# Kernel tuning notes

Measured on AMD Instinct MI355X. Metric: run time of the kernel, lower is better.

## Reference

```python
import jax, jax.numpy as jnp
import numpy as np

EPS = 1e-5
B, T, D, V, NB, C, R, MT = 2, 256, 2048, 32000, 4, 512, 32, 3


def ste_sign_vec(w):
    alpha = jnp.mean(jnp.abs(w))
    hard = alpha * jnp.sign(w)
    hard = jnp.where(hard == 0, alpha, hard)
    return w + jax.lax.stop_gradient(hard - w)


def ste_sign(w):
    alpha = jnp.mean(jnp.abs(w), axis=-1, keepdims=True)
    hard = alpha * jnp.sign(w)
    hard = jnp.where(hard == 0, alpha, hard)
    return w + jax.lax.stop_gradient(hard - w)


def layernorm(x, g, b):
    m = jnp.mean(x, axis=-1, keepdims=True)
    v = jnp.var(x, axis=-1, keepdims=True)
    return (x - m) * jax.lax.rsqrt(v + EPS) * g + b


def hdc_block(x, i, decay_logit, bv_q, bv_k, bv_v, rules, query_bind, logic_gate,
              ln_mem_g, ln_mem_b, ln_attn_g, ln_attn_b, ln_logic_g, ln_logic_b,
              ctrl_ln_g, ctrl_ln_b, down_w, down_b, up_w, up_b):
    t = jnp.arange(T)
    # --- EMA memory (conv1d with decay^k kernel == lower-tri decay matmul) ---
    decay = jax.nn.sigmoid(decay_logit[i])
    expnt = t[:, None] - t[None, :]                     # (T,T)
    A = jnp.where(expnt >= 0, decay ** jnp.maximum(expnt, 0).astype(x.dtype), 0.0)
    mem = jnp.einsum('ts,bsd->btd', A, x)
    x = layernorm(x + mem, ln_mem_g[i], ln_mem_b[i])
    # --- sigmoid-gated boolean causal attention ---
    Q = x * ste_sign_vec(bv_q[i])
    K = x * ste_sign_vec(bv_k[i])
    Vv = x * ste_sign_vec(bv_v[i])
    scores = jnp.einsum('btd,bsd->bts', Q, K) * (D ** -0.5)
    causal = t[:, None] >= t[None, :]
    attn = jnp.where(causal[None], jax.nn.sigmoid(scores * 4.0), 0.0)
    att_out = jnp.einsum('bts,bsd->btd', attn, Vv)
    x = layernorm(x + att_out, ln_attn_g[i], ln_attn_b[i])
    # --- logic layer: sum_r w_r * (x*rule_r) == x * (w @ rules) ---
    rls = ste_sign(rules[i])                            # (R,D)
    query = x * ste_sign_vec(query_bind[i])
    sim = jnp.einsum('btd,rd->btr', query, rls) * (D ** -0.5)
    rw = jax.nn.sigmoid(sim * 4.0)
    logic_out = x * jnp.einsum('btr,rd->btd', rw, rls)
    gate = jax.nn.sigmoid(logic_gate[i])
    x = layernorm(x + gate * (logic_out - x), ln_logic_g[i], ln_logic_b[i])
    # --- controller MLP (dropout inactive in eval) ---
    h = layernorm(x, ctrl_ln_g[i], ctrl_ln_b[i])
    h = jax.nn.gelu(h @ down_w[i].T + down_b[i], approximate=False)
    h = h @ up_w[i].T + up_b[i]
    return x + h


def setup_inputs() -> dict:
    key = jax.random.key(0)
    ks = jax.random.split(key, 12)
    nrm = jax.random.normal
    return {
        'idx': jax.random.randint(ks[0], (B, T), 0, V),
        'codebook': 0.02 * nrm(ks[1], (V, D)),
        'decay_logit': jnp.full((NB,), 2.0),
        'bv_q': 0.5 * nrm(ks[2], (NB, D)),
        'bv_k': 0.5 * nrm(ks[3], (NB, D)),
        'bv_v': 0.5 * nrm(ks[4], (NB, D)),
        'rules': 0.5 * nrm(ks[5], (NB, R, D)),
        'query_bind': 0.5 * nrm(ks[6], (NB, D)),
        'logic_gate': jnp.full((NB,), -1.0),
        'ln_mem_g': jnp.ones((NB, D)), 'ln_mem_b': jnp.zeros((NB, D)),
        'ln_attn_g': jnp.ones((NB, D)), 'ln_attn_b': jnp.zeros((NB, D)),
        'ln_logic_g': jnp.ones((NB, D)), 'ln_logic_b': jnp.zeros((NB, D)),
        'ctrl_ln_g': jnp.ones((NB, D)), 'ctrl_ln_b': jnp.zeros((NB, D)),
        'down_w': nrm(ks[7], (NB, C, D)) / np.sqrt(D), 'down_b': jnp.zeros((NB, C)),
        'up_w': nrm(ks[8], (NB, D, C)) / np.sqrt(C), 'up_b': jnp.zeros((NB, D)),
        'tl_gates': jnp.zeros((MT,)),
        'tl_pos': 0.01 * nrm(ks[9], (MT, D)),
        'tl_ln_g': jnp.ones((D,)), 'tl_ln_b': jnp.zeros((D,)),
        'out_ln_g': jnp.ones((D,)), 'out_ln_b': jnp.zeros((D,)),
        'output_scale': jnp.array(1.0),
    }


def reference(idx, codebook, decay_logit, bv_q, bv_k, bv_v, rules, query_bind,
              logic_gate, ln_mem_g, ln_mem_b, ln_attn_g, ln_attn_b, ln_logic_g,
              ln_logic_b, ctrl_ln_g, ctrl_ln_b, down_w, down_b, up_w, up_b,
              tl_gates, tl_pos, tl_ln_g, tl_ln_b, out_ln_g, out_ln_b, output_scale):
    blk = (decay_logit, bv_q, bv_k, bv_v, rules, query_bind, logic_gate,
           ln_mem_g, ln_mem_b, ln_attn_g, ln_attn_b, ln_logic_g, ln_logic_b,
           ctrl_ln_g, ctrl_ln_b, down_w, down_b, up_w, up_b)

    def run_blocks(h):
        for i in range(NB):
            h = hdc_block(h, i, *blk)
        return h

    # encode: STE bipolar codebook + cyclic permutation positional binding
    tokens = ste_sign(jnp.take(codebook, idx, axis=0))  # (B,T,D)
    perm = (jnp.arange(D)[None, :] - jnp.arange(T)[:, None]) % D  # (T,D)
    tokens = jnp.take_along_axis(tokens, jnp.broadcast_to(perm[None], tokens.shape), axis=2)

    h = run_blocks(tokens)
    for ti in range(1, MT):  # thought loop (n_thoughts = max_thoughts)
        gate = jax.nn.sigmoid(tl_gates[ti])
        thought = run_blocks(layernorm(h, tl_ln_g, tl_ln_b) + tl_pos[ti])
        h = h + gate * (thought - h)

    h = layernorm(h, out_ln_g, out_ln_b)
    logits = (h @ codebook.T) * output_scale  # (B,T,V) weight-tied decoder
    return logits
```

## Files before the change

### kernel.cpp

```cpp
#include <hip/hip_runtime.h>
#include <math.h>

#define TT   256
#define DD   2048
#define VV   32000
#define NBLK 4
#define CC   512
#define RR   32
#define MTT  3
#define NBAT 2
#define NTOK 512

typedef unsigned int u32;
typedef unsigned short ushort_t;
typedef __attribute__((ext_vector_type(8))) short s16x8;
typedef __attribute__((ext_vector_type(4))) float f32x4;

__device__ __forceinline__ float sigm(float x){ return 1.0f/(1.0f+expf(-x)); }

__device__ __forceinline__ ushort_t f2bf(float f){
  u32 u = __float_as_uint(f);
  u32 r = (u + 0x7fffu + ((u >> 16) & 1u)) >> 16;
  return (ushort_t)r;
}
__device__ __forceinline__ float bf2f(ushort_t u){
  return __uint_as_float(((u32)u) << 16);
}

__device__ __forceinline__ void async_copy16(void* lds, const void* g){
  __builtin_amdgcn_global_load_lds((const __attribute__((address_space(1))) u32*)g,
                                   (__attribute__((address_space(3))) u32*)lds, 16, 0, 0);
}

__device__ __forceinline__ float block_sum256(float v){
  #pragma unroll
  for (int off = 32; off > 0; off >>= 1) v += __shfl_down(v, off);
  __shared__ float sh[4];
  __syncthreads();
  if ((threadIdx.x & 63) == 0) sh[threadIdx.x >> 6] = v;
  __syncthreads();
  return sh[0] + sh[1] + sh[2] + sh[3];
}

__global__ __launch_bounds__(256) void cvt2_kernel(const float* __restrict__ a,
    ushort_t* __restrict__ oa, long na4,
    const float* __restrict__ b, ushort_t* __restrict__ ob, long nb4){
  long i = (long)blockIdx.x * 256 + threadIdx.x;
  long stride = (long)gridDim.x * 256;
  long tot = na4 + nb4;
  for (; i < tot; i += stride){
    const float* src = (i < na4) ? a : b;
    ushort_t* dst = (i < na4) ? oa : ob;
    long k = (i < na4) ? i : i - na4;
    float4 v = ((const float4*)src)[k];
    ushort4 o;
    o.x = f2bf(v.x); o.y = f2bf(v.y); o.z = f2bf(v.z); o.w = f2bf(v.w);
    ((ushort4*)dst)[k] = o;
  }
}

__global__ __launch_bounds__(256) void sign_prep_kernel(
    const float* __restrict__ bv_q, const float* __restrict__ bv_k,
    const float* __restrict__ bv_v, const float* __restrict__ query_bind,
    const float* __restrict__ rules, const float* __restrict__ decay_logit,
    float* __restrict__ SQK, float* __restrict__ SV, float* __restrict__ SQB,
    ushort_t* __restrict__ RLSb, ushort_t* __restrict__ Adec){
  int b = blockIdx.x;
  if (b >= 3*NBLK + NBLK*RR){
    int e = b - (3*NBLK + NBLK*RR);
    int i = e >> 8, t = e & (TT - 1), s = threadIdx.x;
    float decay = sigm(decay_logit[i]);
    float l2 = log2f(decay);
    int ex = t - s;
    float v = (ex < 0) ? 0.f : exp2f((float)ex * l2);
    Adec[((size_t)i*TT + t)*TT + s] = f2bf(v);
    return;
  }
  if (b < NBLK){
    const float* q = bv_q + (size_t)b * DD;
    const float* k = bv_k + (size_t)b * DD;
    float sq = 0.f, sk = 0.f;
    #pragma unroll
    for (int j = 0; j < 8; j++){
      int d = threadIdx.x + j*256;
      sq += fabsf(q[d]); sk += fabsf(k[d]);
    }
    float aq = block_sum256(sq) * (1.f/DD);
    float ak = block_sum256(sk) * (1.f/DD);
    float a2 = aq * ak;
    float* o = SQK + (size_t)b * DD;
    #pragma unroll
    for (int j = 0; j < 8; j++){
      int d = threadIdx.x + j*256;
      o[d] = ((q[d] < 0.f) != (k[d] < 0.f)) ? -a2 : a2;
    }
    return;
  }
  const float* w; float* of = nullptr; ushort_t* ob = nullptr;
  if (b < 2*NBLK){ w = bv_v + (size_t)(b - NBLK) * DD; of = SV + (size_t)(b - NBLK) * DD; }
  else if (b < 3*NBLK){ w = query_bind + (size_t)(b - 2*NBLK) * DD; of = SQB + (size_t)(b - 2*NBLK) * DD; }
  else { int r = b - 3*NBLK; w = rules + (size_t)r * DD; ob = RLSb + (size_t)r * DD; }
  float s = 0.f;
  #pragma unroll
  for (int j = 0; j < 8; j++) s += fabsf(w[threadIdx.x + j*256]);
  float a = block_sum256(s) * (1.f/DD);
  #pragma unroll
  for (int j = 0; j < 8; j++){
    int d = threadIdx.x + j*256;
    float v = (w[d] < 0.f) ? -a : a;
    if (of) of[d] = v;
    else    ob[d] = f2bf(v);
  }
}

__global__ __launch_bounds__(256) void encode_kernel(const int* __restrict__ idx,
    const float* __restrict__ cb, float* __restrict__ X, ushort_t* __restrict__ Xrb){
  int token = blockIdx.x;
  int t = token & (TT - 1);
  size_t row = (size_t)idx[token] * DD;
  float s = 0.f;
  #pragma unroll
  for (int j = 0; j < 8; j++) s += fabsf(cb[row + threadIdx.x + j*256]);
  float a = block_sum256(s) * (1.f/DD);
  #pragma unroll
  for (int j = 0; j < 8; j++){
    int d = threadIdx.x + j*256;
    float w = cb[row + ((d - t) & (DD - 1))];
    float v = (w < 0.f) ? -a : a;
    X[(size_t)token * DD + d] = v;
    Xrb[(size_t)token * DD + d] = f2bf(v);
  }
}

__global__ __launch_bounds__(256) void ln_kernel(const float* __restrict__ A,
    const float* __restrict__ g, const float* __restrict__ be,
    float* __restrict__ out, ushort_t* __restrict__ outb,
    const float* __restrict__ qscale, ushort_t* __restrict__ outq,
    const float* __restrict__ vscale, ushort_t* __restrict__ outv){
  size_t row = blockIdx.x;
  const float* a = A + row * DD;
  int d0 = threadIdx.x * 8;
  float v[8];
  *(float4*)&v[0] = *(const float4*)(a + d0);
  *(float4*)&v[4] = *(const float4*)(a + d0 + 4);
  float s = 0.f, ss = 0.f;
  #pragma unroll
  for (int j = 0; j < 8; j++){ s += v[j]; ss += v[j]*v[j]; }
  float mean = block_sum256(s) * (1.f/DD);
  float var  = block_sum256(ss) * (1.f/DD) - mean*mean;
  float inv  = rsqrtf(var + 1e-5f);
  float gv[8], bv[8];
  *(float4*)&gv[0] = *(const float4*)(g + d0);
  *(float4*)&gv[4] = *(const float4*)(g + d0 + 4);
  *(float4*)&bv[0] = *(const float4*)(be + d0);
  *(float4*)&bv[4] = *(const float4*)(be + d0 + 4);
  float y[8];
  #pragma unroll
  for (int j = 0; j < 8; j++) y[j] = (v[j] - mean) * inv * gv[j] + bv[j];
  if (out){
    *(float4*)(out + row*DD + d0)     = *(float4*)&y[0];
    *(float4*)(out + row*DD + d0 + 4) = *(float4*)&y[4];
  }
  if (outb){
    s16x8 o;
    #pragma unroll
    for (int j = 0; j < 8; j++) o[j] = (short)f2bf(y[j]);
    *(s16x8*)(outb + row*DD + d0) = o;
  }
  if (outq){
    float qv[8];
    *(float4*)&qv[0] = *(const float4*)(qscale + d0);
    *(float4*)&qv[4] = *(const float4*)(qscale + d0 + 4);
    s16x8 o;
    #pragma unroll
    for (int j = 0; j < 8; j++) o[j] = (short)f2bf(y[j] * qv[j]);
    *(s16x8*)(outq + row*DD + d0) = o;
  }
  if (outv){
    float vv[8];
    *(float4*)&vv[0] = *(const float4*)(vscale + d0);
    *(float4*)&vv[4] = *(const float4*)(vscale + d0 + 4);
    s16x8 o;
    #pragma unroll
    for (int j = 0; j < 8; j++) o[j] = (short)f2bf(y[j] * vv[j]);
    *(s16x8*)(outv + row*DD + d0) = o;
  }
}

__global__ __launch_bounds__(256) void fuse_logic_kernel(const float* __restrict__ T0,
    const ushort_t* __restrict__ RLSi, const float* __restrict__ SQBi,
    const float* __restrict__ g2, const float* __restrict__ b2,
    const float* __restrict__ gate_ptr,
    const float* __restrict__ g3, const float* __restrict__ b3,
    const float* __restrict__ g4, const float* __restrict__ b4,
    float* __restrict__ X, ushort_t* __restrict__ T1b){
  __shared__ float sh[256*33];
  __shared__ float red[8*32];
  __shared__ float rwsh[32];
  const float RSD = 0.022097086912079608f;
  int tid = threadIdx.x;
  size_t tok = blockIdx.x;
  const float* a = T0 + tok * DD;
  int d0 = tid * 8;
  float v[8];
  *(float4*)&v[0] = *(const float4*)(a + d0);
  *(float4*)&v[4] = *(const float4*)(a + d0 + 4);
  float s = 0.f, ss = 0.f;
  #pragma unroll
  for (int j = 0; j < 8; j++){ s += v[j]; ss += v[j]*v[j]; }
  float mean = block_sum256(s) * (1.f/DD);
  float var  = block_sum256(ss) * (1.f/DD) - mean*mean;
  float inv  = rsqrtf(var + 1e-5f);
  float g2v[8], b2v[8], sqv[8];
  *(float4*)&g2v[0] = *(const float4*)(g2 + d0);
  *(float4*)&g2v[4] = *(const float4*)(g2 + d0 + 4);
  *(float4*)&b2v[0] = *(const float4*)(b2 + d0);
  *(float4*)&b2v[4] = *(const float4*)(b2 + d0 + 4);
  *(float4*)&sqv[0] = *(const float4*)(SQBi + d0);
  *(float4*)&sqv[4] = *(const float4*)(SQBi + d0 + 4);
  float y2[8], xq[8];
  #pragma unroll
  for (int j = 0; j < 8; j++){
    y2[j] = (v[j] - mean) * inv * g2v[j] + b2v[j];
    xq[j] = y2[j] * sqv[j];
  }
  float aa[32];
  #pragma unroll 4
  for (int r = 0; r < 32; r++){
    s16x8 rv = *(const s16x8*)(RLSi + (size_t)r*DD + d0);
    float t = 0.f;
    #pragma unroll
    for (int j = 0; j < 8; j++)
      t = fmaf(xq[j], bf2f((ushort_t)rv[j]), t);
    aa[r] = t;
  }
  #pragma unroll
  for (int r = 0; r < 32; r++) sh[tid*33 + r] = aa[r];
  __syncthreads();
  {
    int r = tid & 31, gg = tid >> 5;
    float t = 0.f;
    #pragma unroll 8
    for (int i = 0; i < 32; i++) t += sh[(gg*32 + i)*33 + r];
    red[gg*32 + r] = t;
  }
  __syncthreads();
  if (tid < 32){
    float t = 0.f;
    #pragma unroll
    for (int gg = 0; gg < 8; gg++) t += red[gg*32 + tid];
    rwsh[tid] = sigm(4.f * RSD * t);
  }
  __syncthreads();
  float gate = sigm(*gate_ptr);
  float acc8[8] = {};
  #pragma unroll 4
  for (int r = 0; r < 32; r++){
    s16x8 rv = *(const s16x8*)(RLSi + (size_t)r*DD + d0);
    float w = rwsh[r];
    #pragma unroll
    for (int j = 0; j < 8; j++)
      acc8[j] = fmaf(w, bf2f((ushort_t)rv[j]), acc8[j]);
  }
  float p3[8]; s = 0.f; ss = 0.f;
  #pragma unroll
  for (int j = 0; j < 8; j++){
    float lo = y2[j] * acc8[j];
    p3[j] = y2[j] + gate * (lo - y2[j]);
    s += p3[j]; ss += p3[j]*p3[j];
  }
  mean = block_sum256(s) * (1.f/DD);
  var  = block_sum256(ss) * (1.f/DD) - mean*mean;
  inv  = rsqrtf(var + 1e-5f);
  float g3v[8], b3v[8];
  *(float4*)&g3v[0] = *(const float4*)(g3 + d0);
  *(float4*)&g3v[4] = *(const float4*)(g3 + d0 + 4);
  *(float4*)&b3v[0] = *(const float4*)(b3 + d0);
  *(float4*)&b3v[4] = *(const float4*)(b3 + d0 + 4);
  float y3[8]; s = 0.f; ss = 0.f;
  #pragma unroll
  for (int j = 0; j < 8; j++){
    y3[j] = (p3[j] - mean) * inv * g3v[j] + b3v[j];
    s += y3[j]; ss += y3[j]*y3[j];
  }
  *(float4*)(X + tok*DD + d0)     = *(float4*)&y3[0];
  *(float4*)(X + tok*DD + d0 + 4) = *(float4*)&y3[4];
  mean = block_sum256(s) * (1.f/DD);
  var  = block_sum256(ss) * (1.f/DD) - mean*mean;
  inv  = rsqrtf(var + 1e-5f);
  float g4v[8], b4v[8];
  *(float4*)&g4v[0] = *(const float4*)(g4 + d0);
  *(float4*)&g4v[4] = *(const float4*)(g4 + d0 + 4);
  *(float4*)&b4v[0] = *(const float4*)(b4 + d0);
  *(float4*)&b4v[4] = *(const float4*)(b4 + d0 + 4);
  s16x8 o;
  #pragma unroll
  for (int j = 0; j < 8; j++)
    o[j] = (short)f2bf((y3[j] - mean) * inv * g4v[j] + b4v[j]);
  *(s16x8*)(T1b + tok*DD + d0) = o;
}

__global__ __launch_bounds__(256) void tl_kernel(const float* __restrict__ Xr,
    float* __restrict__ H, const float* __restrict__ gate_ptr,
    const float* __restrict__ g, const float* __restrict__ be,
    const float* __restrict__ pos,
    float* __restrict__ outX, ushort_t* __restrict__ outXb){
  size_t row = blockIdx.x;
  float gate = gate_ptr ? sigm(*gate_ptr) : 1.f;
  int d0 = threadIdx.x * 8;
  float xr[8];
  *(float4*)&xr[0] = *(const float4*)(Xr + row*DD + d0);
  *(float4*)&xr[4] = *(const float4*)(Xr + row*DD + d0 + 4);
  float v[8]; float s = 0.f, ss = 0.f;
  if (gate_ptr){
    float hv[8];
    *(float4*)&hv[0] = *(const float4*)(H + row*DD + d0);
    *(float4*)&hv[4] = *(const float4*)(H + row*DD + d0 + 4);
    #pragma unroll
    for (int j = 0; j < 8; j++) v[j] = hv[j] + gate * (xr[j] - hv[j]);
  } else {
    #pragma unroll
    for (int j = 0; j < 8; j++) v[j] = xr[j];
  }
  *(float4*)(H + row*DD + d0)     = *(float4*)&v[0];
  *(float4*)(H + row*DD + d0 + 4) = *(float4*)&v[4];
  #pragma unroll
  for (int j = 0; j < 8; j++){ s += v[j]; ss += v[j]*v[j]; }
  float mean = block_sum256(s) * (1.f/DD);
  float var  = block_sum256(ss) * (1.f/DD) - mean*mean;
  float inv  = rsqrtf(var + 1e-5f);
  float gv[8], bv[8];
  *(float4*)&gv[0] = *(const float4*)(g + d0);
  *(float4*)&gv[4] = *(const float4*)(g + d0 + 4);
  *(float4*)&bv[0] = *(const float4*)(be + d0);
  *(float4*)&bv[4] = *(const float4*)(be + d0 + 4);
  float y[8];
  #pragma unroll
  for (int j = 0; j < 8; j++) y[j] = (v[j] - mean) * inv * gv[j] + bv[j];
  if (pos){
    float pv[8];
    *(float4*)&pv[0] = *(const float4*)(pos + d0);
    *(float4*)&pv[4] = *(const float4*)(pos + d0 + 4);
    #pragma unroll
    for (int j = 0; j < 8; j++) y[j] += pv[j];
  }
  if (outX){
    *(float4*)(outX + row*DD + d0)     = *(float4*)&y[0];
    *(float4*)(outX + row*DD + d0 + 4) = *(float4*)&y[4];
  }
  if (outXb){
    s16x8 o;
    #pragma unroll
    for (int j = 0; j < 8; j++) o[j] = (short)f2bf(y[j]);
    *(s16x8*)(outXb + row*DD + d0) = o;
  }
}

template<int BM, int BN, int SPLITK, int ACT, bool CAUSAL, bool OUTBF>
__global__ __launch_bounds__(256) void gemm_nt(const ushort_t* __restrict__ A,
    const ushort_t* __restrict__ B, void* __restrict__ Cv,
    int K, int lda, int ldb, int ldc,
    long sA, long sB, long sC,
    const float* __restrict__ colscale, const float* __restrict__ bias,
    const float* __restrict__ res, ushort_t* __restrict__ mirror,
    const float* __restrict__ alpha_ptr, float alpha_c)
{
  constexpr int FM = BM / 32;
  constexpr int FN = BN / 32;
  __shared__ __align__(16) ushort_t shA[BM * 64];
  __shared__ __align__(16) ushort_t shB[BN * 64];
  const int tid = threadIdx.x;
  const int l = tid & 63, w = tid >> 6;
  const int wr = w >> 1, wc = w & 1;
  const int row0 = blockIdx.y * BM, col0 = blockIdx.x * BN;
  const int zb = blockIdx.z / SPLITK, zk = blockIdx.z % SPLITK;

  if (CAUSAL && col0 > row0 + BM - 1) return;

  A += (size_t)zb * sA;
  B += (size_t)zb * sB;
  const int kbeg = zk * (K / SPLITK), kend = kbeg + K / SPLITK;

  f32x4 acc[FM][FN] = {};

  for (int kt = kbeg; kt < kend; kt += 64){
    #pragma unroll
    for (int i = 0; i < BM/32; i++){
      int o = i*4096 + tid*16;
      int r = o >> 7, c = (o >> 4) & 7;
      int lc = c ^ (r & 7);
      async_copy16((char*)shA + o, A + (size_t)(row0 + r) * lda + kt + lc*8);
    }
    #pragma unroll
    for (int i = 0; i < BN/32; i++){
      int o = i*4096 + tid*16;
      int r = o >> 7, c = (o >> 4) & 7;
      int lc = c ^ (r & 7);
      async_copy16((char*)shB + o, B + (size_t)(col0 + r) * ldb + kt + lc*8);
    }
    __syncthreads();
    #pragma unroll
    for (int kk = 0; kk < 2; kk++){
      s16x8 af[FM], bfr[FN];
      #pragma unroll
      for (int mi = 0; mi < FM; mi++){
        int r = wr*(BM/2) + mi*16 + (l & 15);
        int c = kk*4 + (l >> 4);
        af[mi] = *(const s16x8*)((const char*)shA + r*128 + ((c ^ (r & 7)) << 4));
      }
      #pragma unroll
      for (int ni = 0; ni < FN; ni++){
        int r = wc*(BN/2) + ni*16 + (l & 15);
        int c = kk*4 + (l >> 4);
        bfr[ni] = *(const s16x8*)((const char*)shB + r*128 + ((c ^ (r & 7)) << 4));
      }
      #pragma unroll
      for (int mi = 0; mi < FM; mi++)
        #pragma unroll
        for (int ni = 0; ni < FN; ni++)
          acc[mi][ni] = __builtin_amdgcn_mfma_f32_16x16x32_bf16(af[mi], bfr[ni], acc[mi][ni], 0, 0, 0);
    }
    __syncthreads();
  }

  if (SPLITK > 1){
    float* P = (float*)Cv + (size_t)blockIdx.z * sC;
    #pragma unroll
    for (int mi = 0; mi < FM; mi++)
      #pragma unroll
      for (int ni = 0; ni < FN; ni++)
        #pragma unroll
        for (int j = 0; j < 4; j++){
          int m = row0 + wr*(BM/2) + mi*16 + (l >> 4)*4 + j;
          int n = col0 + wc*(BN/2) + ni*16 + (l & 15);
          P[(size_t)m * ldc + n] = acc[mi][ni][j];
        }
    return;
  }

  float alpha = alpha_c * (alpha_ptr ? *alpha_ptr : 1.f);
  float* Cf = (float*)Cv + (size_t)zb * sC;
  ushort_t* Cb = (ushort_t*)Cv + (size_t)zb * sC;
  const float* resz = res ? res + (size_t)zb * sC : nullptr;
  #pragma unroll
  for (int mi = 0; mi < FM; mi++){
    #pragma unroll
    for (int ni = 0; ni < FN; ni++){
      #pragma unroll
      for (int j = 0; j < 4; j++){
        int m = row0 + wr*(BM/2) + mi*16 + (l >> 4)*4 + j;
        int n = col0 + wc*(BN/2) + ni*16 + (l & 15);
        float v = acc[mi][ni][j] * alpha;
        if (colscale) v *= colscale[n];
        if (bias) v += bias[n];
        if (ACT == 1) v = sigm(4.f * v);
        else if (ACT == 2) v = 0.5f * v * (1.f + erff(v * 0.70710678118654752f));
        if (CAUSAL && n > m) v = 0.f;
        if (resz) v += resz[(size_t)m * ldc + n];
        if (OUTBF) Cb[(size_t)m * ldc + n] = f2bf(v);
        else       Cf[(size_t)m * ldc + n] = v;
        if (mirror) mirror[(size_t)m * ldc + n] = f2bf(v);
      }
    }
  }
}

__global__ __launch_bounds__(256) void gemm_nn(const ushort_t* __restrict__ A,
    const ushort_t* __restrict__ B, float* __restrict__ C,
    int K, int lda, int ldb, int ldc,
    long sA, long sB, long sC,
    const float* __restrict__ res, int tri)
{
  __shared__ __align__(16) ushort_t shA[64 * 64];
  __shared__ __align__(16) ushort_t shB[64 * 64];
  const int tid = threadIdx.x;
  const int l = tid & 63, w = tid >> 6;
  const int wr = w >> 1, wc = w & 1;
  const int row0 = blockIdx.y * 64, col0 = blockIdx.x * 64;
  A += (size_t)blockIdx.z * sA;
  B += (size_t)blockIdx.z * sB;

  const int kb = tid & 63;
  const int nb0 = (tid >> 6) * 8;
  const int kend = tri ? (row0 + 64 < K ? row0 + 64 : K) : K;

  f32x4 acc[2][2] = {};

  for (int kt = 0; kt < kend; kt += 64){
    #pragma unroll
    for (int i = 0; i < 2; i++){
      int o = i*4096 + tid*16;
      int r = o >> 7, c = (o >> 4) & 7;
      int lc = c ^ (r & 7);
      async_copy16((char*)shA + o, A + (size_t)(row0 + r) * lda + kt + lc*8);
    }
    #pragma unroll
    for (int i = 0; i < 2; i++){
      int n0 = nb0 + i*32;
      s16x8 v = *(const s16x8*)(B + (size_t)(kt + kb) * ldb + col0 + n0);
      #pragma unroll
      for (int j = 0; j < 8; j++){
        int n = n0 + j;
        int off = n*128 + (((kb >> 3) ^ (n & 7)) << 4) + ((kb & 7) << 1);
        *(ushort_t*)((char*)shB + off) = (ushort_t)v[j];
      }
    }
    __syncthreads();
    #pragma unroll
    for (int kk = 0; kk < 2; kk++){
      s16x8 af[2], bfr[2];
      #pragma unroll
      for (int mi = 0; mi < 2; mi++){
        int r = wr*32 + mi*16 + (l & 15);
        int c = kk*4 + (l >> 4);
        af[mi] = *(const s16x8*)((const char*)shA + r*128 + ((c ^ (r & 7)) << 4));
      }
      #pragma unroll
      for (int ni = 0; ni < 2; ni++){
        int r = wc*32 + ni*16 + (l & 15);
        int c = kk*4 + (l >> 4);
        bfr[ni] = *(const s16x8*)((const char*)shB + r*128 + ((c ^ (r & 7)) << 4));
      }
      #pragma unroll
      for (int mi = 0; mi < 2; mi++)
        #pragma unroll
        for (int ni = 0; ni < 2; ni++)
          acc[mi][ni] = __builtin_amdgcn_mfma_f32_16x16x32_bf16(af[mi], bfr[ni], acc[mi][ni], 0, 0, 0);
    }
    __syncthreads();
  }

  float* Cf = C + (size_t)blockIdx.z * sC;
  const float* resz = res ? res + (size_t)blockIdx.z * sC : nullptr;
  #pragma unroll
  for (int mi = 0; mi < 2; mi++)
    #pragma unroll
    for (int ni = 0; ni < 2; ni++)
      #pragma unroll
      for (int j = 0; j < 4; j++){
        int m = row0 + wr*32 + mi*16 + (l >> 4)*4 + j;
        int n = col0 + wc*32 + ni*16 + (l & 15);
        float v = acc[mi][ni][j];
        if (resz) v += resz[(size_t)m * ldc + n];
        Cf[(size_t)m * ldc + n] = v;
      }
}

template<int S, int ACT, bool CAUSAL, bool OUTBF>
__global__ __launch_bounds__(256) void reduce_epi(const float* __restrict__ P,
    void* __restrict__ outv, int M, int N, const float* __restrict__ bias, float alpha){
  long MN = (long)M * N;
  long idx = ((long)blockIdx.x * 256 + threadIdx.x) * 4;
  int b = (int)(idx / MN);
  long r = idx - (long)b * MN;
  int m = (int)(r / N), n = (int)(r % N);
  if (CAUSAL && n > m){
    if (OUTBF){ ushort4 z = {0,0,0,0}; *(ushort4*)&((ushort_t*)outv)[(long)b*MN + r] = z; }
    else      { float4 z = {0.f,0.f,0.f,0.f}; *(float4*)&((float*)outv)[(long)b*MN + r] = z; }
    return;
  }
  float vv[4] = {0.f, 0.f, 0.f, 0.f};
  #pragma unroll
  for (int s = 0; s < S; s++){
    float4 p = *(const float4*)&P[((long)(b*S + s)) * MN + r];
    vv[0] += p.x; vv[1] += p.y; vv[2] += p.z; vv[3] += p.w;
  }
  ushort4 ob; float4 of;
  float* po = (float*)&of;
  ushort_t* pb = (ushort_t*)&ob;
  #pragma unroll
  for (int j = 0; j < 4; j++){
    float v = vv[j] * alpha;
    if (bias) v += bias[n + j];
    if (ACT == 1) v = sigm(4.f * v);
    else if (ACT == 2) v = 0.5f * v * (1.f + erff(v * 0.70710678118654752f));
    if (CAUSAL && n + j > m) v = 0.f;
    po[j] = v; pb[j] = f2bf(v);
  }
  if (OUTBF) *(ushort4*)&((ushort_t*)outv)[(long)b*MN + r] = ob;
  else       *(float4*)&((float*)outv)[(long)b*MN + r] = of;
}

__global__ __launch_bounds__(256) void gemm_ntf(const ushort_t* __restrict__ A,
    const float* __restrict__ B, float* __restrict__ C,
    const float* __restrict__ alpha_ptr)
{
  constexpr int BM = 256, BN = 64, FM = 8, FN = 2;
  constexpr int NXB = VV / BN;
  __shared__ __align__(16) ushort_t shA[BM * 64];
  __shared__ __align__(16) ushort_t shB[BN * 64];
  const int tid = threadIdx.x;
  const int l = tid & 63, w = tid >> 6;
  const int wr = w >> 1, wc = w & 1;
  int bid = blockIdx.x;
  int swz = (bid & 7) * 125 + (bid >> 3);
  int bx = swz % NXB, by = swz / NXB;
  const int row0 = by * BM, col0 = bx * BN;

  f32x4 acc[FM][FN] = {};

  for (int kt = 0; kt < DD; kt += 64){
    #pragma unroll
    for (int i = 0; i < FM; i++){
      int o = i*4096 + tid*16;
      int r = o >> 7, c = (o >> 4) & 7;
      int lc = c ^ (r & 7);
      async_copy16((char*)shA + o, A + (size_t)(row0 + r) * DD + kt + lc*8);
    }
    #pragma unroll
    for (int i = 0; i < 4; i++){
      int idx4 = tid + i*256;
      int r = idx4 >> 4, kq = idx4 & 15;
      float4 v = *(const float4*)(B + (size_t)(col0 + r) * DD + kt + kq*4);
      u32 p0 = ((u32)f2bf(v.y) << 16) | (u32)f2bf(v.x);
      u32 p1 = ((u32)f2bf(v.w) << 16) | (u32)f2bf(v.z);
      int off = r*128 + (((kq >> 1) ^ (r & 7)) << 4) + ((kq & 1) << 3);
      uint2 pp; pp.x = p0; pp.y = p1;
      *(uint2*)((char*)shB + off) = pp;
    }
    __syncthreads();
    #pragma unroll
    for (int kk = 0; kk < 2; kk++){
      s16x8 af[FM], bfr[FN];
      #pragma unroll
      for (int mi = 0; mi < FM; mi++){
        int r = wr*(BM/2) + mi*16 + (l & 15);
        int c = kk*4 + (l >> 4);
        af[mi] = *(const s16x8*)((const char*)shA + r*128 + ((c ^ (r & 7)) << 4));
      }
      #pragma unroll
      for (int ni = 0; ni < FN; ni++){
        int r = wc*(BN/2) + ni*16 + (l & 15);
        int c = kk*4 + (l >> 4);
        bfr[ni] = *(const s16x8*)((const char*)shB + r*128 + ((c ^ (r & 7)) << 4));
      }
      #pragma unroll
      for (int mi = 0; mi < FM; mi++)
        #pragma unroll
        for (int ni = 0; ni < FN; ni++)
          acc[mi][ni] = __builtin_amdgcn_mfma_f32_16x16x32_bf16(af[mi], bfr[ni], acc[mi][ni], 0, 0, 0);
    }
    __syncthreads();
  }

  float alpha = *alpha_ptr;
  #pragma unroll
  for (int mi = 0; mi < FM; mi++)
    #pragma unroll
    for (int ni = 0; ni < FN; ni++)
      #pragma unroll
      for (int j = 0; j < 4; j++){
        int m = row0 + wr*(BM/2) + mi*16 + (l >> 4)*4 + j;
        int n = col0 + wc*(BN/2) + ni*16 + (l & 15);
        C[(size_t)m * VV + n] = acc[mi][ni][j] * alpha;
      }
}

extern "C" void kernel_launch(void* const* d_in, const int* in_sizes, int n_in,
                              void* d_out, int out_size, void* d_ws, size_t ws_size,
                              hipStream_t stream){
  const int*   idx        = (const int*)  d_in[0];
  const float* cb         = (const float*)d_in[1];
  const float* decay_lg   = (const float*)d_in[2];
  const float* bv_q       = (const float*)d_in[3];
  const float* bv_k       = (const float*)d_in[4];
  const float* bv_v       = (const float*)d_in[5];
  const float* rules      = (const float*)d_in[6];
  const float* query_bind = (const float*)d_in[7];
  const float* logic_gate = (const float*)d_in[8];
  const float* ln_mem_g   = (const float*)d_in[9];
  const float* ln_mem_b   = (const float*)d_in[10];
  const float* ln_attn_g  = (const float*)d_in[11];
  const float* ln_attn_b  = (const float*)d_in[12];
  const float* ln_logic_g = (const float*)d_in[13];
  const float* ln_logic_b = (const float*)d_in[14];
  const float* ctrl_g     = (const float*)d_in[15];
  const float* ctrl_b     = (const float*)d_in[16];
  const float* down_w     = (const float*)d_in[17];
  const float* down_b     = (const float*)d_in[18];
  const float* up_w       = (const float*)d_in[19];
  const float* up_b       = (const float*)d_in[20];
  const float* tl_gates   = (const float*)d_in[21];
  const float* tl_pos     = (const float*)d_in[22];
  const float* tl_g       = (const float*)d_in[23];
  const float* tl_b       = (const float*)d_in[24];
  const float* out_g      = (const float*)d_in[25];
  const float* out_b      = (const float*)d_in[26];
  const float* oscale     = (const float*)d_in[27];
  float* out = (float*)d_out;

  const size_t ND = (size_t)NTOK * DD;
  char* p = (char*)d_ws;
  auto alloc = [&](size_t bytes){ void* r = p; p += (bytes + 255) & ~(size_t)255; return r; };
  float*    X       = (float*)   alloc(ND * 4);
  float*    H       = (float*)   alloc(ND * 4);
  float*    T0      = (float*)   alloc(ND * 4);
  ushort_t* Xrb     = (ushort_t*)alloc(ND * 2);
  ushort_t* Xb      = (ushort_t*)alloc(ND * 2);
  ushort_t* Xqb     = (ushort_t*)alloc(ND * 2);
  ushort_t* Xvb     = (ushort_t*)alloc(ND * 2);
  ushort_t* T1b     = (ushort_t*)alloc(ND * 2);
  ushort_t* ATTNb   = (ushort_t*)alloc((size_t)NBAT * TT * TT * 2);
  ushort_t* CBbuf   = (ushort_t*)alloc((size_t)NTOK * CC * 2);
  float*    PP      = (float*)   alloc((size_t)8 * NTOK * CC * 4);
  float*    SQK     = (float*)   alloc((size_t)NBLK * DD * 4);
  float*    SV      = (float*)   alloc((size_t)NBLK * DD * 4);
  float*    SQB     = (float*)   alloc((size_t)NBLK * DD * 4);
  ushort_t* RLSb    = (ushort_t*)alloc((size_t)NBLK * RR * DD * 2);
  ushort_t* Adec    = (ushort_t*)alloc((size_t)NBLK * TT * TT * 2);
  ushort_t* down_wb = (ushort_t*)alloc((size_t)NBLK * CC * DD * 2);
  ushort_t* up_wb   = (ushort_t*)alloc((size_t)NBLK * DD * CC * 2);

  const float RSD = 0.022097086912079608f;

  sign_prep_kernel<<<3*NBLK + NBLK*RR + NBLK*TT, 256, 0, stream>>>(
      bv_q, bv_k, bv_v, query_bind, rules, decay_lg, SQK, SV, SQB, RLSb, Adec);
  cvt2_kernel<<<2048, 256, 0, stream>>>(down_w, down_wb, (long)NBLK*CC*DD/4,
                                        up_w, up_wb, (long)NBLK*DD*CC/4);
  encode_kernel<<<NTOK, 256, 0, stream>>>(idx, cb, X, Xrb);

  auto run_blocks = [&](){
    for (int i = 0; i < NBLK; i++){
      const size_t iD = (size_t)i * DD;
      gemm_nn<<<dim3(DD/64, TT/64, NBAT), 256, 0, stream>>>(
          Adec + (size_t)i*TT*TT, Xrb, T0, TT, TT, DD, DD,
          0, (long)TT*DD, (long)TT*DD, X, 1);
      ln_kernel<<<NTOK, 256, 0, stream>>>(T0, ln_mem_g + iD, ln_mem_b + iD,
          X, Xb, SQK + iD, Xqb, SV + iD, Xvb);
      gemm_nt<64,64,8,0,true,false><<<dim3(TT/64, TT/64, NBAT*8), 256, 0, stream>>>(
          Xqb, Xb, PP, DD, DD, DD, TT,
          (long)TT*DD, (long)TT*DD, (long)TT*TT,
          nullptr, nullptr, nullptr, nullptr, nullptr, 1.f);
      reduce_epi<8,1,true,true><<<(NBAT*TT*TT)/1024, 256, 0, stream>>>(
          PP, ATTNb, TT, TT, nullptr, RSD);
      gemm_nn<<<dim3(DD/64, TT/64, NBAT), 256, 0, stream>>>(
          ATTNb, Xvb, T0, TT, TT, DD, DD,
          (long)TT*TT, (long)TT*DD, (long)TT*DD, X, 1);
      fuse_logic_kernel<<<NTOK, 256, 0, stream>>>(T0,
          RLSb + (size_t)i*RR*DD, SQB + iD,
          ln_attn_g + iD, ln_attn_b + iD, logic_gate + i,
          ln_logic_g + iD, ln_logic_b + iD, ctrl_g + iD, ctrl_b + iD,
          X, T1b);
      gemm_nt<64,64,8,0,false,false><<<dim3(CC/64, NTOK/64, 8), 256, 0, stream>>>(
          T1b, down_wb + (size_t)i*CC*DD, PP, DD, DD, DD, CC,
          0, 0, (long)NTOK*CC,
          nullptr, nullptr, nullptr, nullptr, nullptr, 1.f);
      reduce_epi<8,2,false,true><<<(NTOK*CC)/1024, 256, 0, stream>>>(
          PP, CBbuf, NTOK, CC, down_b + (size_t)i*CC, 1.f);
      gemm_nt<64,64,1,0,false,false><<<dim3(DD/64, NTOK/64, 1), 256, 0, stream>>>(
          CBbuf, up_wb + (size_t)i*DD*CC, X, CC, CC, CC, DD,
          0, 0, 0, nullptr, up_b + iD, X, Xrb, nullptr, 1.f);
    }
  };

  run_blocks();
  tl_kernel<<<NTOK, 256, 0, stream>>>(X, H, nullptr, tl_g, tl_b,
      tl_pos + (size_t)1*DD, X, Xrb);
  run_blocks();
  tl_kernel<<<NTOK, 256, 0, stream>>>(X, H, tl_gates + 1, tl_g, tl_b,
      tl_pos + (size_t)2*DD, X, Xrb);
  run_blocks();
  tl_kernel<<<NTOK, 256, 0, stream>>>(X, H, tl_gates + 2, out_g, out_b,
      nullptr, nullptr, T1b);
  gemm_ntf<<<(VV/64)*(NTOK/256), 256, 0, stream>>>(T1b, cb, out, oscale);
}
```

Before: 1.057 ms.

## Fuse split-K GEMMs with their reductions using cooperative grid sync

The split-K scores GEMM and the down-projection GEMM each get their partial-sum reduction and epilogue (sigmoid with causal mask, or bias plus GELU) folded into the same kernel. The two stages are separated by a cooperative-groups grid barrier, and the kernels are launched with hipLaunchCooperativeKernel. This removes one kernel launch and its inter-kernel gap per fused pair, 24 launches in total across the forward pass. In exchange it adds a grid-wide sync, requires the whole grid (up to 512 blocks) to be co-resident, and cooperative launches can carry their own overhead.

```diff
diff --git a/kernel.cpp b/kernel.cpp
--- a/kernel.cpp
+++ b/kernel.cpp
@@ -1,5 +1,8 @@
 #include <hip/hip_runtime.h>
+#include <hip/hip_cooperative_groups.h>
 #include <math.h>
+
+namespace cg = cooperative_groups;
 
 #define TT   256
 #define DD   2048
@@ -17,6 +20,9 @@
 typedef __attribute__((ext_vector_type(4))) float f32x4;
 
 __device__ __forceinline__ float sigm(float x){ return 1.0f/(1.0f+expf(-x)); }
+__device__ __forceinline__ float gelu(float v){
+  return 0.5f * v * (1.f + erff(v * 0.70710678118654752f));
+}
 
 __device__ __forceinline__ ushort_t f2bf(float f){
   u32 u = __float_as_uint(f);
@@ -356,14 +362,13 @@
   }
 }
 
-template<int BM, int BN, int SPLITK, int ACT, bool CAUSAL, bool OUTBF>
+template<int BM, int BN, int ACT, bool OUTBF>
 __global__ __launch_bounds__(256) void gemm_nt(const ushort_t* __restrict__ A,
     const ushort_t* __restrict__ B, void* __restrict__ Cv,
     int K, int lda, int ldb, int ldc,
     long sA, long sB, long sC,
-    const float* __restrict__ colscale, const float* __restrict__ bias,
-    const float* __restrict__ res, ushort_t* __restrict__ mirror,
-    const float* __restrict__ alpha_ptr, float alpha_c)
+    const float* __restrict__ bias,
+    const float* __restrict__ res, ushort_t* __restrict__ mirror)
 {
   constexpr int FM = BM / 32;
   constexpr int FN = BN / 32;
@@ -373,17 +378,14 @@
   const int l = tid & 63, w = tid >> 6;
   const int wr = w >> 1, wc = w & 1;
   const int row0 = blockIdx.y * BM, col0 = blockIdx.x * BN;
-  const int zb = blockIdx.z / SPLITK, zk = blockIdx.z % SPLITK;
-
-  if (CAUSAL && col0 > row0 + BM - 1) return;
+  const int zb = blockIdx.z;
 
   A += (size_t)zb * sA;
   B += (size_t)zb * sB;
-  const int kbeg = zk * (K / SPLITK), kend = kbeg + K / SPLITK;
 
   f32x4 acc[FM][FN] = {};
 
-  for (int kt = kbeg; kt < kend; kt += 64){
+  for (int kt = 0; kt < K; kt += 64){
     #pragma unroll
     for (int i = 0; i < BM/32; i++){
       int o = i*4096 + tid*16;
@@ -423,22 +425,6 @@
     __syncthreads();
   }
 
-  if (SPLITK > 1){
-    float* P = (float*)Cv + (size_t)blockIdx.z * sC;
-    #pragma unroll
-    for (int mi = 0; mi < FM; mi++)
-      #pragma unroll
-      for (int ni = 0; ni < FN; ni++)
-        #pragma unroll
-        for (int j = 0; j < 4; j++){
-          int m = row0 + wr*(BM/2) + mi*16 + (l >> 4)*4 + j;
-          int n = col0 + wc*(BN/2) + ni*16 + (l & 15);
-          P[(size_t)m * ldc + n] = acc[mi][ni][j];
-        }
-    return;
-  }
-
-  float alpha = alpha_c * (alpha_ptr ? *alpha_ptr : 1.f);
   float* Cf = (float*)Cv + (size_t)zb * sC;
   ushort_t* Cb = (ushort_t*)Cv + (size_t)zb * sC;
   const float* resz = res ? res + (size_t)zb * sC : nullptr;
@@ -450,12 +436,9 @@
       for (int j = 0; j < 4; j++){
         int m = row0 + wr*(BM/2) + mi*16 + (l >> 4)*4 + j;
         int n = col0 + wc*(BN/2) + ni*16 + (l & 15);
-        float v = acc[mi][ni][j] * alpha;
-        if (colscale) v *= colscale[n];
+        float v = acc[mi][ni][j];
         if (bias) v += bias[n];
-        if (ACT == 1) v = sigm(4.f * v);
-        else if (ACT == 2) v = 0.5f * v * (1.f + erff(v * 0.70710678118654752f));
-        if (CAUSAL && n > m) v = 0.f;
+        if (ACT == 2) v = gelu(v);
         if (resz) v += resz[(size_t)m * ldc + n];
         if (OUTBF) Cb[(size_t)m * ldc + n] = f2bf(v);
         else       Cf[(size_t)m * ldc + n] = v;
@@ -546,39 +529,197 @@
       }
 }
 
-template<int S, int ACT, bool CAUSAL, bool OUTBF>
-__global__ __launch_bounds__(256) void reduce_epi(const float* __restrict__ P,
-    void* __restrict__ outv, int M, int N, const float* __restrict__ bias, float alpha){
-  long MN = (long)M * N;
-  long idx = ((long)blockIdx.x * 256 + threadIdx.x) * 4;
-  int b = (int)(idx / MN);
-  long r = idx - (long)b * MN;
-  int m = (int)(r / N), n = (int)(r % N);
-  if (CAUSAL && n > m){
-    if (OUTBF){ ushort4 z = {0,0,0,0}; *(ushort4*)&((ushort_t*)outv)[(long)b*MN + r] = z; }
-    else      { float4 z = {0.f,0.f,0.f,0.f}; *(float4*)&((float*)outv)[(long)b*MN + r] = z; }
-    return;
-  }
-  float vv[4] = {0.f, 0.f, 0.f, 0.f};
-  #pragma unroll
-  for (int s = 0; s < S; s++){
-    float4 p = *(const float4*)&P[((long)(b*S + s)) * MN + r];
-    vv[0] += p.x; vv[1] += p.y; vv[2] += p.z; vv[3] += p.w;
-  }
-  ushort4 ob; float4 of;
-  float* po = (float*)&of;
-  ushort_t* pb = (ushort_t*)&ob;
-  #pragma unroll
-  for (int j = 0; j < 4; j++){
-    float v = vv[j] * alpha;
-    if (bias) v += bias[n + j];
-    if (ACT == 1) v = sigm(4.f * v);
-    else if (ACT == 2) v = 0.5f * v * (1.f + erff(v * 0.70710678118654752f));
-    if (CAUSAL && n + j > m) v = 0.f;
-    po[j] = v; pb[j] = f2bf(v);
-  }
-  if (OUTBF) *(ushort4*)&((ushort_t*)outv)[(long)b*MN + r] = ob;
-  else       *(float4*)&((float*)outv)[(long)b*MN + r] = of;
+__global__ __launch_bounds__(256) void scores_fused(
+    const ushort_t* __restrict__ Aq, const ushort_t* __restrict__ Bx,
+    float* __restrict__ P, ushort_t* __restrict__ OUT, float alpha)
+{
+  __shared__ __align__(16) ushort_t shA[64 * 64];
+  __shared__ __align__(16) ushort_t shB[64 * 64];
+  const int tid = threadIdx.x;
+  const int l = tid & 63, w = tid >> 6;
+  const int wr = w >> 1, wc = w & 1;
+  const int row0 = blockIdx.y * 64, col0 = blockIdx.x * 64;
+  const int z = blockIdx.z, zb = z >> 3, zk = z & 7;
+
+  if (col0 <= row0 + 63){
+    const ushort_t* A = Aq + (size_t)zb * TT * DD;
+    const ushort_t* B = Bx + (size_t)zb * TT * DD;
+    const int kbeg = zk * (DD/8);
+    f32x4 acc[2][2] = {};
+    for (int kt = kbeg; kt < kbeg + DD/8; kt += 64){
+      #pragma unroll
+      for (int i = 0; i < 2; i++){
+        int o = i*4096 + tid*16;
+        int r = o >> 7, c = (o >> 4) & 7;
+        int lc = c ^ (r & 7);
+        async_copy16((char*)shA + o, A + (size_t)(row0 + r) * DD + kt + lc*8);
+      }
+      #pragma unroll
+      for (int i = 0; i < 2; i++){
+        int o = i*4096 + tid*16;
+        int r = o >> 7, c = (o >> 4) & 7;
+        int lc = c ^ (r & 7);
+        async_copy16((char*)shB + o, B + (size_t)(col0 + r) * DD + kt + lc*8);
+      }
+      __syncthreads();
+      #pragma unroll
+      for (int kk = 0; kk < 2; kk++){
+        s16x8 af[2], bfr[2];
+        #pragma unroll
+        for (int mi = 0; mi < 2; mi++){
+          int r = wr*32 + mi*16 + (l & 15);
+          int c = kk*4 + (l >> 4);
+          af[mi] = *(const s16x8*)((const char*)shA + r*128 + ((c ^ (r & 7)) << 4));
+        }
+        #pragma unroll
+        for (int ni = 0; ni < 2; ni++){
+          int r = wc*32 + ni*16 + (l & 15);
+          int c = kk*4 + (l >> 4);
+          bfr[ni] = *(const s16x8*)((const char*)shB + r*128 + ((c ^ (r & 7)) << 4));
+        }
+        #pragma unroll
+        for (int mi = 0; mi < 2; mi++)
+          #pragma unroll
+          for (int ni = 0; ni < 2; ni++)
+            acc[mi][ni] = __builtin_amdgcn_mfma_f32_16x16x32_bf16(af[mi], bfr[ni], acc[mi][ni], 0, 0, 0);
+      }
+      __syncthreads();
+    }
+    float* Pz = P + (size_t)z * TT * TT;
+    #pragma unroll
+    for (int mi = 0; mi < 2; mi++)
+      #pragma unroll
+      for (int ni = 0; ni < 2; ni++)
+        #pragma unroll
+        for (int j = 0; j < 4; j++){
+          int m = row0 + wr*32 + mi*16 + (l >> 4)*4 + j;
+          int n = col0 + wc*32 + ni*16 + (l & 15);
+          Pz[(size_t)m * TT + n] = acc[mi][ni][j];
+        }
+  }
+
+  cg::this_grid().sync();
+
+  const long MN = (long)TT * TT;
+  long gid = (((long)blockIdx.z * 4 + blockIdx.y) * 4 + blockIdx.x) * 256 + tid;
+  long nq = (NBAT * MN) / 4;
+  if (gid < nq){
+    long idx = gid * 4;
+    int b = (int)(idx / MN);
+    long r = idx - (long)b * MN;
+    int m = (int)(r / TT), n = (int)(r % TT);
+    ushort4 ob;
+    if (n > m){
+      ob.x = 0; ob.y = 0; ob.z = 0; ob.w = 0;
+    } else {
+      float vv[4] = {0.f, 0.f, 0.f, 0.f};
+      #pragma unroll
+      for (int s = 0; s < 8; s++){
+        float4 p4 = *(const float4*)&P[((long)(b*8 + s)) * MN + r];
+        vv[0] += p4.x; vv[1] += p4.y; vv[2] += p4.z; vv[3] += p4.w;
+      }
+      ushort_t* pb = (ushort_t*)&ob;
+      #pragma unroll
+      for (int j = 0; j < 4; j++){
+        float v = sigm(4.f * (vv[j] * alpha));
+        if (n + j > m) v = 0.f;
+        pb[j] = f2bf(v);
+      }
+    }
+    *(ushort4*)&OUT[(long)b * MN + r] = ob;
+  }
+}
+
+__global__ __launch_bounds__(256) void down_fused(
+    const ushort_t* __restrict__ At, const ushort_t* __restrict__ Bw,
+    float* __restrict__ P, ushort_t* __restrict__ OUT, const float* __restrict__ bias)
+{
+  __shared__ __align__(16) ushort_t shA[64 * 64];
+  __shared__ __align__(16) ushort_t shB[64 * 64];
+  const int tid = threadIdx.x;
+  const int l = tid & 63, w = tid >> 6;
+  const int wr = w >> 1, wc = w & 1;
+  const int row0 = blockIdx.y * 64, col0 = blockIdx.x * 64;
+  const int zk = blockIdx.z;
+
+  {
+    const int kbeg = zk * (DD/8);
+    f32x4 acc[2][2] = {};
+    for (int kt = kbeg; kt < kbeg + DD/8; kt += 64){
+      #pragma unroll
+      for (int i = 0; i < 2; i++){
+        int o = i*4096 + tid*16;
+        int r = o >> 7, c = (o >> 4) & 7;
+        int lc = c ^ (r & 7);
+        async_copy16((char*)shA + o, At + (size_t)(row0 + r) * DD + kt + lc*8);
+      }
+      #pragma unroll
+      for (int i = 0; i < 2; i++){
+        int o = i*4096 + tid*16;
+        int r = o >> 7, c = (o >> 4) & 7;
+        int lc = c ^ (r & 7);
+        async_copy16((char*)shB + o, Bw + (size_t)(col0 + r) * DD + kt + lc*8);
+      }
+      __syncthreads();
+      #pragma unroll
+      for (int kk = 0; kk < 2; kk++){
+        s16x8 af[2], bfr[2];
+        #pragma unroll
+        for (int mi = 0; mi < 2; mi++){
+          int r = wr*32 + mi*16 + (l & 15);
+          int c = kk*4 + (l >> 4);
+          af[mi] = *(const s16x8*)((const char*)shA + r*128 + ((c ^ (r & 7)) << 4));
+        }
+        #pragma unroll
+        for (int ni = 0; ni < 2; ni++){
+          int r = wc*32 + ni*16 + (l & 15);
+          int c = kk*4 + (l >> 4);
+          bfr[ni] = *(const s16x8*)((const char*)shB + r*128 + ((c ^ (r & 7)) << 4));
+        }
+        #pragma unroll
+        for (int mi = 0; mi < 2; mi++)
+          #pragma unroll
+          for (int ni = 0; ni < 2; ni++)
+            acc[mi][ni] = __builtin_amdgcn_mfma_f32_16x16x32_bf16(af[mi], bfr[ni], acc[mi][ni], 0, 0, 0);
+      }
+      __syncthreads();
+    }
+    float* Pz = P + (size_t)zk * NTOK * CC;
+    #pragma unroll
+    for (int mi = 0; mi < 2; mi++)
+      #pragma unroll
+      for (int ni = 0; ni < 2; ni++)
+        #pragma unroll
+        for (int j = 0; j < 4; j++){
+          int m = row0 + wr*32 + mi*16 + (l >> 4)*4 + j;
+          int n = col0 + wc*32 + ni*16 + (l & 15);
+          Pz[(size_t)m * CC + n] = acc[mi][ni][j];
+        }
+  }
+
+  cg::this_grid().sync();
+
+  const long MN = (long)NTOK * CC;
+  long gid = (((long)blockIdx.z * 8 + blockIdx.y) * 8 + blockIdx.x) * 256 + tid;
+  long nq = MN / 4;
+  if (gid < nq){
+    long r = gid * 4;
+    int n = (int)(r % CC);
+    float vv[4] = {0.f, 0.f, 0.f, 0.f};
+    #pragma unroll
+    for (int s = 0; s < 8; s++){
+      float4 p4 = *(const float4*)&P[(long)s * MN + r];
+      vv[0] += p4.x; vv[1] += p4.y; vv[2] += p4.z; vv[3] += p4.w;
+    }
+    ushort4 ob;
+    ushort_t* pb = (ushort_t*)&ob;
+    #pragma unroll
+    for (int j = 0; j < 4; j++){
+      float v = gelu(vv[j] + bias[n + j]);
+      pb[j] = f2bf(v);
+    }
+    *(ushort4*)&OUT[r] = ob;
+  }
 }
 
 __global__ __launch_bounds__(256) void gemm_ntf(const ushort_t* __restrict__ A,
@@ -702,7 +843,8 @@
   ushort_t* T1b     = (ushort_t*)alloc(ND * 2);
   ushort_t* ATTNb   = (ushort_t*)alloc((size_t)NBAT * TT * TT * 2);
   ushort_t* CBbuf   = (ushort_t*)alloc((size_t)NTOK * CC * 2);
-  float*    PP      = (float*)   alloc((size_t)8 * NTOK * CC * 4);
+  float*    PP      = (float*)   alloc((size_t)16 * TT * TT * 4);
+  float*    PD      = (float*)   alloc((size_t)8 * NTOK * CC * 4);
   float*    SQK     = (float*)   alloc((size_t)NBLK * DD * 4);
   float*    SV      = (float*)   alloc((size_t)NBLK * DD * 4);
   float*    SQB     = (float*)   alloc((size_t)NBLK * DD * 4);
@@ -727,12 +869,13 @@
           0, (long)TT*DD, (long)TT*DD, X, 1);
       ln_kernel<<<NTOK, 256, 0, stream>>>(T0, ln_mem_g + iD, ln_mem_b + iD,
           X, Xb, SQK + iD, Xqb, SV + iD, Xvb);
-      gemm_nt<64,64,8,0,true,false><<<dim3(TT/64, TT/64, NBAT*8), 256, 0, stream>>>(
-          Xqb, Xb, PP, DD, DD, DD, TT,
-          (long)TT*DD, (long)TT*DD, (long)TT*TT,
-          nullptr, nullptr, nullptr, nullptr, nullptr, 1.f);
-      reduce_epi<8,1,true,true><<<(NBAT*TT*TT)/1024, 256, 0, stream>>>(
-          PP, ATTNb, TT, TT, nullptr, RSD);
+      {
+        const ushort_t* a0 = Xqb; const ushort_t* a1 = Xb;
+        float* a2 = PP; ushort_t* a3 = ATTNb; float a4 = RSD;
+        void* args[] = { &a0, &a1, &a2, &a3, &a4 };
+        hipLaunchCooperativeKernel((const void*)scores_fused,
+            dim3(TT/64, TT/64, NBAT*8), dim3(256), args, 0, stream);
+      }
       gemm_nn<<<dim3(DD/64, TT/64, NBAT), 256, 0, stream>>>(
           ATTNb, Xvb, T0, TT, TT, DD, DD,
           (long)TT*TT, (long)TT*DD, (long)TT*DD, X, 1);
@@ -741,15 +884,16 @@
           ln_attn_g + iD, ln_attn_b + iD, logic_gate + i,
           ln_logic_g + iD, ln_logic_b + iD, ctrl_g + iD, ctrl_b + iD,
           X, T1b);
-      gemm_nt<64,64,8,0,false,false><<<dim3(CC/64, NTOK/64, 8), 256, 0, stream>>>(
-          T1b, down_wb + (size_t)i*CC*DD, PP, DD, DD, DD, CC,
-          0, 0, (long)NTOK*CC,
-          nullptr, nullptr, nullptr, nullptr, nullptr, 1.f);
-      reduce_epi<8,2,false,true><<<(NTOK*CC)/1024, 256, 0, stream>>>(
-          PP, CBbuf, NTOK, CC, down_b + (size_t)i*CC, 1.f);
-      gemm_nt<64,64,1,0,false,false><<<dim3(DD/64, NTOK/64, 1), 256, 0, stream>>>(
+      {
+        const ushort_t* a0 = T1b; const ushort_t* a1 = down_wb + (size_t)i*CC*DD;
+        float* a2 = PD; ushort_t* a3 = CBbuf; const float* a4 = down_b + (size_t)i*CC;
+        void* args[] = { &a0, &a1, &a2, &a3, &a4 };
+        hipLaunchCooperativeKernel((const void*)down_fused,
+            dim3(CC/64, NTOK/64, 8), dim3(256), args, 0, stream);
+      }
+      gemm_nt<64,64,0,false><<<dim3(DD/64, NTOK/64, 1), 256, 0, stream>>>(
           CBbuf, up_wb + (size_t)i*DD*CC, X, CC, CC, CC, DD,
-          0, 0, 0, nullptr, up_b + iD, X, Xrb, nullptr, 1.f);
+          0, 0, 0, up_b + iD, X, Xrb);
     }
   };
 
```

Result: slower. 2.442 ms (+131.0%).
